# Performance work log

Measured on AMD Instinct MI355X. Metric: run time of the kernel, lower is better.

Reference implementation:

```python
import jax, jax.numpy as jnp
import numpy as np
import math

NUM_CLASSES = 15
IN_CH = 256
FEAT_CH = 256
STRIDES = (8, 16, 32, 64, 128)
SCALES = (4.0,)
RATIOS = (6.0,)
ANGLES = (-0.125 * math.pi, 0.125 * math.pi, 0.375 * math.pi, 0.625 * math.pi)
NUM_ANCHORS = len(SCALES) * len(RATIOS) * len(ANGLES)  # 4
WH_RATIO_CLIP = 1e-6


def conv2d(x, w, b, pad):
    y = jax.lax.conv_general_dilated(
        x, w, window_strides=(1, 1), padding=[(pad, pad), (pad, pad)],
        dimension_numbers=("NCHW", "OIHW", "NCHW"))
    return y + b[None, :, None, None]


def gen_grid_anchors(base_size, feat_h, feat_w, stride):
    # AnchorGeneratorRotated (S2ANet style): base anchors [A,5] = (xc,yc,w,h,angle)
    scales = jnp.asarray(SCALES, jnp.float32)
    ratios = jnp.asarray(RATIOS, jnp.float32)
    angles = jnp.asarray(ANGLES, jnp.float32)
    h_ratios = jnp.sqrt(ratios)
    w_ratios = 1.0 / h_ratios
    ones = jnp.ones_like(angles)
    ws = (base_size * w_ratios[:, None, None] * scales[None, :, None] * ones[None, None, :]).reshape(-1)
    hs = (base_size * h_ratios[:, None, None] * scales[None, :, None] * ones[None, None, :]).reshape(-1)
    ang = jnp.tile(angles, ratios.size * scales.size)
    ctr = 0.5 * (base_size - 1.0)
    base = jnp.stack([jnp.full_like(ws, ctr), jnp.full_like(ws, ctr), ws, hs, ang], axis=-1)  # [A,5]
    xx = jnp.arange(feat_w, dtype=jnp.float32) * stride
    yy = jnp.arange(feat_h, dtype=jnp.float32) * stride
    gx, gy = jnp.meshgrid(xx, yy)  # [H,W]
    zeros = jnp.zeros_like(gx)
    shift = jnp.stack([gx, gy, zeros, zeros, zeros], axis=-1)  # [H,W,5]
    return base[None, None] + shift[:, :, None, :]  # [H,W,A,5]


def norm_angle(a):
    # normalize to [-pi/4, 3pi/4)
    return (a + 0.25 * jnp.pi) % jnp.pi - 0.25 * jnp.pi


def rboxes_decode(anchors, deltas):
    # is_encode_relative=False branch of delta2rbox
    max_ratio = abs(math.log(WH_RATIO_CLIP))
    dx, dy, dw, dh, da = jnp.split(deltas, 5, axis=-1)
    rx, ry, rw, rh, ra = jnp.split(anchors, 5, axis=-1)
    dw = jnp.clip(dw, -max_ratio, max_ratio)
    dh = jnp.clip(dh, -max_ratio, max_ratio)
    gx = dx * rw + rx
    gy = dy * rh + ry
    gw = rw * jnp.exp(dw)
    gh = rh * jnp.exp(dh)
    ga = norm_angle(da + ra)
    return jnp.concatenate([gx, gy, gw, gh, ga], axis=-1)


def _head_level(x, stride, p):
    B, _, H, W = x.shape
    # reg tower (2 stacked 3x3 conv + relu)
    r = jax.nn.relu(conv2d(x, p["reg_w0"], p["reg_b0"], 1))
    r = jax.nn.relu(conv2d(r, p["reg_w1"], p["reg_b1"], 1))
    bbox = conv2d(r, p["reg_head_w"], p["reg_head_b"], 0)
    bbox = bbox.transpose(0, 2, 3, 1).reshape(B, H, W, NUM_ANCHORS, 5)
    conf = conv2d(r, p["conf_w"], p["conf_b"], 0)
    conf = conf.transpose(0, 2, 3, 1).reshape(B, H, W, NUM_ANCHORS, 1)
    anchors = gen_grid_anchors(float(stride), H, W, float(stride))  # [H,W,A,5]
    dec = rboxes_decode(anchors[None], jax.lax.stop_gradient(bbox))  # [B,H,W,A,5]
    # refine-anchor selection: pick decoded box of max-confidence anchor per location
    conf_sig = jax.nn.sigmoid(jax.lax.stop_gradient(conf))[..., 0]  # [B,H,W,A]
    idx = jnp.argmax(conf_sig, axis=3)  # [B,H,W]
    refine = jnp.take_along_axis(dec, idx[..., None, None], axis=3)[:, :, :, 0, :]  # [B,H,W,5]
    # cls tower
    c = jax.nn.relu(conv2d(x, p["cls_w0"], p["cls_b0"], 1))
    c = jax.nn.relu(conv2d(c, p["cls_w1"], p["cls_b1"], 1))
    cls = conv2d(c, p["cls_head_w"], p["cls_head_b"], 0)
    cls = cls.transpose(0, 2, 3, 1).reshape(B, H, W, NUM_ANCHORS, NUM_CLASSES)
    # per-image scores as in get_bboxes: sigmoid(cls) * sigmoid(conf)
    scores = jax.nn.sigmoid(cls.reshape(B, -1, NUM_CLASSES)) * jax.nn.sigmoid(conf.reshape(B, -1, 1))
    return scores, dec.reshape(B, -1, 5), refine


def setup_inputs() -> dict:
    key = jax.random.key(0)
    ks = jax.random.split(key, 24)
    B = 8
    sizes = [(128, 128), (64, 64), (32, 32), (16, 16), (8, 8)]
    inp = {}
    for i, (h, w) in enumerate(sizes):
        inp[f"feat{i}"] = jax.random.normal(ks[i], (B, IN_CH, h, w), jnp.float32)
    std = 0.01
    bias_cls = float(-np.log((1 - 0.01) / 0.01))
    inp["reg_w0"] = jax.random.normal(ks[5], (FEAT_CH, IN_CH, 3, 3), jnp.float32) * std
    inp["reg_b0"] = jnp.zeros((FEAT_CH,), jnp.float32)
    inp["reg_w1"] = jax.random.normal(ks[6], (FEAT_CH, FEAT_CH, 3, 3), jnp.float32) * std
    inp["reg_b1"] = jnp.zeros((FEAT_CH,), jnp.float32)
    inp["cls_w0"] = jax.random.normal(ks[7], (FEAT_CH, IN_CH, 3, 3), jnp.float32) * std
    inp["cls_b0"] = jnp.zeros((FEAT_CH,), jnp.float32)
    inp["cls_w1"] = jax.random.normal(ks[8], (FEAT_CH, FEAT_CH, 3, 3), jnp.float32) * std
    inp["cls_b1"] = jnp.zeros((FEAT_CH,), jnp.float32)
    inp["reg_head_w"] = jax.random.normal(ks[9], (5 * NUM_ANCHORS, FEAT_CH, 1, 1), jnp.float32) * std
    inp["reg_head_b"] = jnp.zeros((5 * NUM_ANCHORS,), jnp.float32)
    inp["cls_head_w"] = jax.random.normal(ks[10], (NUM_CLASSES * NUM_ANCHORS, FEAT_CH, 1, 1), jnp.float32) * std
    inp["cls_head_b"] = jnp.full((NUM_CLASSES * NUM_ANCHORS,), bias_cls, jnp.float32)
    inp["conf_w"] = jax.random.normal(ks[11], (NUM_ANCHORS, FEAT_CH, 1, 1), jnp.float32) * std
    inp["conf_b"] = jnp.full((NUM_ANCHORS,), bias_cls, jnp.float32)
    return inp


def reference(feat0, feat1, feat2, feat3, feat4,
              reg_w0, reg_b0, reg_w1, reg_b1,
              cls_w0, cls_b0, cls_w1, cls_b1,
              reg_head_w, reg_head_b, cls_head_w, cls_head_b,
              conf_w, conf_b):
    p = dict(reg_w0=reg_w0, reg_b0=reg_b0, reg_w1=reg_w1, reg_b1=reg_b1,
             cls_w0=cls_w0, cls_b0=cls_b0, cls_w1=cls_w1, cls_b1=cls_b1,
             reg_head_w=reg_head_w, reg_head_b=reg_head_b,
             cls_head_w=cls_head_w, cls_head_b=cls_head_b,
             conf_w=conf_w, conf_b=conf_b)
    feats = [feat0, feat1, feat2, feat3, feat4]
    scores_ls, boxes_ls = [], []
    for x, s in zip(feats, STRIDES):
        sc, bx, _ = _head_level(x, s, p)
        scores_ls.append(sc)
        boxes_ls.append(bx)
    scores = jnp.concatenate(scores_ls, axis=1)  # [B, N_total, num_classes]
    boxes = jnp.concatenate(boxes_ls, axis=1)    # [B, N_total, 5]
    return scores, boxes
```

## Files before the change

kernel.cpp:

```cpp
#include <hip/hip_runtime.h>


typedef __attribute__((ext_vector_type(8))) _Float16 f16x8;
typedef __attribute__((ext_vector_type(4))) float f32x4;

#define SCORES_TOTAL 10475520ull

__device__ __forceinline__ unsigned short f2h(float f) {
  union { _Float16 h; unsigned short u; } x;
  x.h = (_Float16)f;
  return x.u;
}

__device__ __forceinline__ float sigmf(float x) {
  return 1.0f / (1.0f + expf(-x));
}

__device__ __forceinline__ void gload_lds16(const unsigned short* g,
                                            unsigned short* l) {
  __builtin_amdgcn_global_load_lds(
      (const __attribute__((address_space(1))) unsigned int*)g,
      (__attribute__((address_space(3))) unsigned int*)l, 16, 0, 0);
}

__device__ __forceinline__ void lvl_lookup(int gm, int& logW, int& mbase) {
  if (gm < 131072) { logW = 7; mbase = 0; }
  else if (gm < 163840) { logW = 6; mbase = 131072; }
  else if (gm < 172032) { logW = 5; mbase = 163840; }
  else if (gm < 174080) { logW = 4; mbase = 172032; }
  else { logW = 3; mbase = 174080; }
}

__global__ __launch_bounds__(256) void prep_convw(
    const float* __restrict__ w0, const float* __restrict__ w1,
    const float* __restrict__ w2, const float* __restrict__ w3,
    unsigned short* __restrict__ wtout) {
  int g = blockIdx.x * 256 + threadIdx.x;
  int q = g >> 16;
  int wsel = q / 9;
  int kk = q - wsel * 9;
  int r = g & 65535;
  int oc = r >> 8, ic = r & 255;
  const float* src = (wsel == 0) ? w0 : (wsel == 1) ? w1 : (wsel == 2) ? w2 : w3;
  float v = src[(size_t)(oc * 256 + ic) * 9 + kk];
  wtout[(size_t)wsel * 589824 + (size_t)((kk << 8) + oc) * 256 + ic] = f2h(v);
}

__global__ __launch_bounds__(256) void prep_small(
    const float* __restrict__ clsh, const float* __restrict__ regh,
    const float* __restrict__ confw,
    unsigned short* __restrict__ wc, unsigned short* __restrict__ wh,
    unsigned short* __restrict__ zp) {
  int g = blockIdx.x * 256 + threadIdx.x;
  if (g < 16384) {
    int row = g >> 8, ic = g & 255;
    float v = (row < 60) ? clsh[row * 256 + ic] : 0.0f;
    wc[g] = f2h(v);
  } else if (g < 24576) {
    int gg = g - 16384;
    int row = gg >> 8, ic = gg & 255;
    float v = 0.0f;
    if (row < 20) v = regh[row * 256 + ic];
    else if (row < 24) v = confw[(row - 20) * 256 + ic];
    wh[gg] = f2h(v);
  } else if (g < 24640) {
    zp[g - 24576] = 0;
  }
}

__global__ __launch_bounds__(256) void to_nhwc_all(
    const float* __restrict__ f0, const float* __restrict__ f1,
    const float* __restrict__ f2, const float* __restrict__ f3,
    const float* __restrict__ f4, unsigned short* __restrict__ out) {
  __shared__ unsigned short L[64][258];
  const int t = threadIdx.x;
  const int gm0 = blockIdx.x * 64;
  int logW, mbase;
  const float* in;
  if (gm0 < 131072) { logW = 7; mbase = 0; in = f0; }
  else if (gm0 < 163840) { logW = 6; mbase = 131072; in = f1; }
  else if (gm0 < 172032) { logW = 5; mbase = 163840; in = f2; }
  else if (gm0 < 174080) { logW = 4; mbase = 172032; in = f3; }
  else { logW = 3; mbase = 174080; in = f4; }
  const int logHW = 2 * logW;
  const int HW = 1 << logHW;
  const int lm0 = gm0 - mbase;
  const int b = lm0 >> logHW;
  const int hw0 = lm0 & (HW - 1);
#pragma unroll
  for (int it = 0; it < 16; ++it) {
    int c = it * 16 + (t >> 4);
    int j4 = (t & 15) * 4;
    float4 v = *reinterpret_cast<const float4*>(
        in + (size_t)(b * 256 + c) * HW + hw0 + j4);
    L[j4 + 0][c] = f2h(v.x);
    L[j4 + 1][c] = f2h(v.y);
    L[j4 + 2][c] = f2h(v.z);
    L[j4 + 3][c] = f2h(v.w);
  }
  __syncthreads();
#pragma unroll
  for (int it = 0; it < 16; ++it) {
    int j = it * 4 + (t >> 6);
    int c4 = (t & 63) * 4;
    unsigned v0 = (unsigned)L[j][c4 + 0] | ((unsigned)L[j][c4 + 1] << 16);
    unsigned v1 = (unsigned)L[j][c4 + 2] | ((unsigned)L[j][c4 + 3] << 16);
    uint2 v = make_uint2(v0, v1);
    *reinterpret_cast<uint2*>(out + ((size_t)(gm0 + j) << 8) + c4) = v;
  }
}

__global__ __launch_bounds__(256, 2) void conv1f(
    const unsigned short* __restrict__ xin,
    const unsigned short* __restrict__ wtR,
    const unsigned short* __restrict__ wtC,
    const float* __restrict__ biasR, const float* __restrict__ biasC,
    const unsigned short* __restrict__ zp,
    unsigned short* __restrict__ outR,
    unsigned short* __restrict__ outC, int gm_base) {
  __shared__ unsigned short pool[24576];
  const int t = threadIdx.x;
  const int lane = t & 63;
  const int wv = t >> 6;
  const int wm = wv >> 1, wn = wv & 1;
  const int gm0 = gm_base + blockIdx.x * 128;
  const int n0 = blockIdx.y << 7;
  int logW, mbase;
  lvl_lookup(gm0, logW, mbase);
  const int logHW = 2 * logW;
  const int H = 1 << logW, W = H;
  const int HWm1 = (1 << logHW) - 1, Wm1 = W - 1;

  const int srow = lane >> 2;
  const int schk = (((lane & 3) ^ ((lane >> 3) & 3)) << 3);
  int hjj[2], wjj[2];
  const unsigned short* aptrj[2];
  const unsigned short* bRj[2];
  const unsigned short* bCj[2];
  const int sldrow = (wv << 5);
#pragma unroll
  for (int j = 0; j < 2; ++j) {
    int gm = gm0 + sldrow + (j << 4) + srow;
    int lm = gm - mbase;
    int hw = lm & HWm1;
    hjj[j] = hw >> logW;
    wjj[j] = hw & Wm1;
    aptrj[j] = xin + ((size_t)gm << 8) + schk;
    int br = n0 + sldrow + (j << 4) + srow;
    bRj[j] = wtR + ((size_t)br << 8) + schk;
    bCj[j] = wtC + ((size_t)br << 8) + schk;
  }

  f32x4 accR[4][4], accC[4][4];
#pragma unroll
  for (int i = 0; i < 4; ++i)
#pragma unroll
    for (int j = 0; j < 4; ++j) {
      accR[i][j] = (f32x4){0.f, 0.f, 0.f, 0.f};
      accC[i][j] = (f32x4){0.f, 0.f, 0.f, 0.f};
    }

  const int arow = (wm << 6) + (lane & 15);
  const int brow = (wn << 6) + (lane & 15);
  const int sxor = ((lane & 15) >> 1) & 3;
  const int achk = (((lane >> 4) ^ sxor) << 3);

  {
    const int moff = (-W - 1) << 8;
#pragma unroll
    for (int j = 0; j < 2; ++j) {
      bool valid = (hjj[j] > 0) & (wjj[j] > 0);
      const unsigned short* g = valid ? (aptrj[j] + moff) : zp;
      gload_lds16(g, pool + ((sldrow + (j << 4)) << 5));
    }
#pragma unroll
    for (int j = 0; j < 2; ++j) {
      gload_lds16(bRj[j], pool + 8192 + ((sldrow + (j << 4)) << 5));
      gload_lds16(bCj[j], pool + 16384 + ((sldrow + (j << 4)) << 5));
    }
  }

  int cur = 0;
#pragma unroll 1
  for (int ph = 0; ph < 72; ++ph) {
    asm volatile("s_waitcnt vmcnt(0)" ::: "memory");
    __builtin_amdgcn_s_barrier();
    __builtin_amdgcn_sched_barrier(0);
    if (ph < 71) {
      const int p = ph + 1;
      const int kk = p >> 3;
      const int k3 = kk / 3;
      const int dy = k3 - 1, dxv = kk - k3 * 3 - 1;
      const int moff = ((dy << logW) + dxv) << 8;
      const int ic0 = (p & 7) << 5;
      const int nb = (cur ^ 1) << 12;
      const int bko = (kk << 16) + ic0;
#pragma unroll
      for (int j = 0; j < 2; ++j) {
        bool valid = ((unsigned)(hjj[j] + dy) < (unsigned)H) &
                     ((unsigned)(wjj[j] + dxv) < (unsigned)W);
        const unsigned short* g = valid ? (aptrj[j] + moff + ic0) : zp;
        gload_lds16(g, pool + nb + ((sldrow + (j << 4)) << 5));
      }
#pragma unroll
      for (int j = 0; j < 2; ++j) {
        gload_lds16(bRj[j] + bko, pool + 8192 + nb + ((sldrow + (j << 4)) << 5));
        gload_lds16(bCj[j] + bko, pool + 16384 + nb + ((sldrow + (j << 4)) << 5));
      }
    }
    const int cb = cur << 12;
    f16x8 a[4], bR[4], bC[4];
#pragma unroll
    for (int mf = 0; mf < 4; ++mf)
      a[mf] = *reinterpret_cast<const f16x8*>(
          pool + cb + ((arow + (mf << 4)) << 5) + achk);
#pragma unroll
    for (int nf = 0; nf < 4; ++nf) {
      bR[nf] = *reinterpret_cast<const f16x8*>(
          pool + 8192 + cb + ((brow + (nf << 4)) << 5) + achk);
      bC[nf] = *reinterpret_cast<const f16x8*>(
          pool + 16384 + cb + ((brow + (nf << 4)) << 5) + achk);
    }
#pragma unroll
    for (int mf = 0; mf < 4; ++mf)
#pragma unroll
      for (int nf = 0; nf < 4; ++nf) {
        accR[mf][nf] = __builtin_amdgcn_mfma_f32_16x16x32_f16(
            a[mf], bR[nf], accR[mf][nf], 0, 0, 0);
        accC[mf][nf] = __builtin_amdgcn_mfma_f32_16x16x32_f16(
            a[mf], bC[nf], accC[mf][nf], 0, 0, 0);
      }
    cur ^= 1;
  }
  __syncthreads();

  const int erow = t >> 1;
  const int ech = t & 1;
  const unsigned short* esrc =
      pool + ((((erow >> 6) << 1) + ech) << 12) + ((erow & 63) << 6);
  unsigned short* ep = pool + (wv << 12);
  const int eg = (lane >> 4) << 2;
  const int el = lane & 15;
  const int lrow0 = gm0 - gm_base;

#pragma unroll
  for (int nf = 0; nf < 4; ++nf) {
    float bi = biasR[n0 + (wn << 6) + (nf << 4) + el];
#pragma unroll
    for (int mf = 0; mf < 4; ++mf)
#pragma unroll
      for (int r = 0; r < 4; ++r)
        ep[((mf << 4) + eg + r) * 64 + (nf << 4) + el] =
            f2h(fmaxf(accR[mf][nf][r] + bi, 0.0f));
  }
  __syncthreads();
  {
    unsigned short* edst =
        outR + ((size_t)(lrow0 + erow) << 8) + n0 + (ech << 6);
#pragma unroll
    for (int q = 0; q < 8; ++q)
      reinterpret_cast<uint4*>(edst)[q] =
          reinterpret_cast<const uint4*>(esrc)[q];
  }
  __syncthreads();
#pragma unroll
  for (int nf = 0; nf < 4; ++nf) {
    float bi = biasC[n0 + (wn << 6) + (nf << 4) + el];
#pragma unroll
    for (int mf = 0; mf < 4; ++mf)
#pragma unroll
      for (int r = 0; r < 4; ++r)
        ep[((mf << 4) + eg + r) * 64 + (nf << 4) + el] =
            f2h(fmaxf(accC[mf][nf][r] + bi, 0.0f));
  }
  __syncthreads();
  {
    unsigned short* edst =
        outC + ((size_t)(lrow0 + erow) << 8) + n0 + (ech << 6);
#pragma unroll
    for (int q = 0; q < 8; ++q)
      reinterpret_cast<uint4*>(edst)[q] =
          reinterpret_cast<const uint4*>(esrc)[q];
  }
}

__global__ __launch_bounds__(256, 2) void conv2w(
    const unsigned short* __restrict__ xin,
    const unsigned short* __restrict__ wt,
    const float* __restrict__ bias,
    const unsigned short* __restrict__ zp,
    unsigned short* __restrict__ yout,
    int gm_base) {
  __shared__ unsigned short pool[24576];
  const int t = threadIdx.x;
  const int lane = t & 63;
  const int wv = t >> 6;
  const int wm = wv >> 1, wn = wv & 1;
  const int gm0 = gm_base + blockIdx.x * 128;
  int logW, mbase;
  lvl_lookup(gm0, logW, mbase);
  const int logHW = 2 * logW;
  const int H = 1 << logW, W = H;
  const int HWm1 = (1 << logHW) - 1, Wm1 = W - 1;

  const int srow = lane >> 2;
  const int schk = (((lane & 3) ^ ((lane >> 3) & 3)) << 3);
  int hjj[2], wjj[2];
  const unsigned short* aptrj[2];
  const int sldrow = (wv << 5);
#pragma unroll
  for (int j = 0; j < 2; ++j) {
    int gm = gm0 + sldrow + (j << 4) + srow;
    int lm = gm - mbase;
    int hw = lm & HWm1;
    hjj[j] = hw >> logW;
    wjj[j] = hw & Wm1;
    aptrj[j] = xin + ((size_t)(gm - gm_base) << 8) + schk;
  }
  const unsigned short* bpj[4];
#pragma unroll
  for (int j = 0; j < 4; ++j) {
    int row = (wv << 6) + (j << 4) + srow;
    bpj[j] = wt + ((size_t)row << 8) + schk;
  }

  f32x4 acc[4][8];
#pragma unroll
  for (int i = 0; i < 4; ++i)
#pragma unroll
    for (int j = 0; j < 8; ++j) acc[i][j] = (f32x4){0.f, 0.f, 0.f, 0.f};

  const int arow = (wm << 6) + (lane & 15);
  const int brow = (wn << 7) + (lane & 15);
  const int sxor = ((lane & 15) >> 1) & 3;
  const int achk = (((lane >> 4) ^ sxor) << 3);

  {
    const int moff = (-W - 1) << 8;
#pragma unroll
    for (int j = 0; j < 2; ++j) {
      bool valid = (hjj[j] > 0) & (wjj[j] > 0);
      const unsigned short* g = valid ? (aptrj[j] + moff) : zp;
      gload_lds16(g, pool + ((sldrow + (j << 4)) << 5));
    }
#pragma unroll
    for (int j = 0; j < 4; ++j)
      gload_lds16(bpj[j], pool + 8192 + (((wv << 6) + (j << 4)) << 5));
  }

  int cur = 0;
#pragma unroll 1
  for (int ph = 0; ph < 72; ++ph) {
    asm volatile("s_waitcnt vmcnt(0)" ::: "memory");
    __builtin_amdgcn_s_barrier();
    __builtin_amdgcn_sched_barrier(0);
    if (ph < 71) {
      const int p = ph + 1;
      const int kk = p >> 3;
      const int k3 = kk / 3;
      const int dy = k3 - 1, dxv = kk - k3 * 3 - 1;
      const int moff = ((dy << logW) + dxv) << 8;
      const int ic0 = (p & 7) << 5;
      const int bko = (kk << 16) + ic0;
#pragma unroll
      for (int j = 0; j < 2; ++j) {
        bool valid = ((unsigned)(hjj[j] + dy) < (unsigned)H) &
                     ((unsigned)(wjj[j] + dxv) < (unsigned)W);
        const unsigned short* g = valid ? (aptrj[j] + moff + ic0) : zp;
        gload_lds16(g, pool + ((cur ^ 1) << 12) + ((sldrow + (j << 4)) << 5));
      }
#pragma unroll
      for (int j = 0; j < 4; ++j)
        gload_lds16(bpj[j] + bko, pool + 8192 + ((cur ^ 1) << 13) +
                                      (((wv << 6) + (j << 4)) << 5));
    }
    const int cbA = cur << 12;
    const int cbB = cur << 13;
    f16x8 a[4], b[8];
#pragma unroll
    for (int mf = 0; mf < 4; ++mf)
      a[mf] = *reinterpret_cast<const f16x8*>(
          pool + cbA + ((arow + (mf << 4)) << 5) + achk);
#pragma unroll
    for (int nf = 0; nf < 8; ++nf)
      b[nf] = *reinterpret_cast<const f16x8*>(
          pool + 8192 + cbB + ((brow + (nf << 4)) << 5) + achk);
#pragma unroll
    for (int mf = 0; mf < 4; ++mf)
#pragma unroll
      for (int nf = 0; nf < 8; ++nf)
        acc[mf][nf] = __builtin_amdgcn_mfma_f32_16x16x32_f16(
            a[mf], b[nf], acc[mf][nf], 0, 0, 0);
    cur ^= 1;
  }
  __syncthreads();

  const int erow = t >> 1;
  const int ech = t & 1;
  const unsigned short* esrc =
      pool + ((((erow >> 6) << 1) + ech) << 12) + ((erow & 63) << 6);
  unsigned short* ep = pool + (wv << 12);
  const int eg = (lane >> 4) << 2;
  const int el = lane & 15;

#pragma unroll
  for (int h = 0; h < 2; ++h) {
    if (h) __syncthreads();
#pragma unroll
    for (int q4 = 0; q4 < 4; ++q4) {
      int nf = (h << 2) + q4;
      float bi = bias[(wn << 7) + (nf << 4) + el];
#pragma unroll
      for (int mf = 0; mf < 4; ++mf)
#pragma unroll
        for (int r = 0; r < 4; ++r)
          ep[((mf << 4) + eg + r) * 64 + (q4 << 4) + el] =
              f2h(fmaxf(acc[mf][nf][r] + bi, 0.0f));
    }
    __syncthreads();
    unsigned short* edst =
        yout + ((size_t)(gm0 + erow) << 8) + (ech << 7) + (h << 6);
#pragma unroll
    for (int q = 0; q < 8; ++q)
      reinterpret_cast<uint4*>(edst)[q] =
          reinterpret_cast<const uint4*>(esrc)[q];
  }
}

__global__ __launch_bounds__(256) void head24_mfma(
    const unsigned short* __restrict__ t2,
    const unsigned short* __restrict__ wh,
    const float* __restrict__ regb, const float* __restrict__ confb,
    float* __restrict__ hbuf) {
  const int t = threadIdx.x, lane = t & 63, wv = t >> 6;
  const int rowb = blockIdx.x * 256 + wv * 64;
  const int kgrp = (lane >> 4) << 3;
  const int l15 = lane & 15;
  f32x4 acc[4][2];
#pragma unroll
  for (int i = 0; i < 4; ++i)
#pragma unroll
    for (int j = 0; j < 2; ++j) acc[i][j] = (f32x4){0.f, 0.f, 0.f, 0.f};
#pragma unroll
  for (int k0 = 0; k0 < 256; k0 += 32) {
    f16x8 a[4], b[2];
#pragma unroll
    for (int mf = 0; mf < 4; ++mf)
      a[mf] = *reinterpret_cast<const f16x8*>(
          t2 + (((size_t)(rowb + (mf << 4) + l15)) << 8) + k0 + kgrp);
#pragma unroll
    for (int nf = 0; nf < 2; ++nf)
      b[nf] = *reinterpret_cast<const f16x8*>(
          wh + (size_t)(((nf << 4) + l15) << 8) + k0 + kgrp);
#pragma unroll
    for (int mf = 0; mf < 4; ++mf)
#pragma unroll
      for (int nf = 0; nf < 2; ++nf)
        acc[mf][nf] = __builtin_amdgcn_mfma_f32_16x16x32_f16(
            a[mf], b[nf], acc[mf][nf], 0, 0, 0);
  }
#pragma unroll
  for (int nf = 0; nf < 2; ++nf) {
    int c = (nf << 4) + l15;
    if (c < 24) {
      float bi = (c < 20) ? regb[c] : confb[c - 20];
#pragma unroll
      for (int mf = 0; mf < 4; ++mf)
#pragma unroll
        for (int r = 0; r < 4; ++r) {
          int m = rowb + (mf << 4) + ((lane >> 4) << 2) + r;
          hbuf[(size_t)m * 24 + c] = acc[mf][nf][r] + bi;
        }
    }
  }
}

__global__ __launch_bounds__(256) void cls_scores(
    const unsigned short* __restrict__ t2,
    const unsigned short* __restrict__ wcw,
    const float* __restrict__ clsb,
    const float* __restrict__ hbuf,
    float* __restrict__ outs, int gm_base) {
  const int t = threadIdx.x, lane = t & 63, wv = t >> 6;
  const int gm0 = gm_base + blockIdx.x * 256;
  int logW, mbase, lvl_off;
  if (gm0 < 131072) { logW = 7; mbase = 0; lvl_off = 0; }
  else if (gm0 < 163840) { logW = 6; mbase = 131072; lvl_off = 65536; }
  else if (gm0 < 172032) { logW = 5; mbase = 163840; lvl_off = 81920; }
  else if (gm0 < 174080) { logW = 4; mbase = 172032; lvl_off = 86016; }
  else { logW = 3; mbase = 174080; lvl_off = 87040; }
  const int logHW = 2 * logW, HWm1 = (1 << logHW) - 1;
  const int rowb = gm0 + wv * 64;
  const int kgrp = (lane >> 4) << 3;
  const int l15 = lane & 15;
  f32x4 acc[4][4];
#pragma unroll
  for (int i = 0; i < 4; ++i)
#pragma unroll
    for (int j = 0; j < 4; ++j) acc[i][j] = (f32x4){0.f, 0.f, 0.f, 0.f};
#pragma unroll
  for (int k0 = 0; k0 < 256; k0 += 32) {
    f16x8 a[4], b[4];
#pragma unroll
    for (int mf = 0; mf < 4; ++mf)
      a[mf] = *reinterpret_cast<const f16x8*>(
          t2 + (((size_t)(rowb + (mf << 4) + l15)) << 8) + k0 + kgrp);
#pragma unroll
    for (int nf = 0; nf < 4; ++nf)
      b[nf] = *reinterpret_cast<const f16x8*>(
          wcw + (size_t)(((nf << 4) + l15) << 8) + k0 + kgrp);
#pragma unroll
    for (int mf = 0; mf < 4; ++mf)
#pragma unroll
      for (int nf = 0; nf < 4; ++nf)
        acc[mf][nf] = __builtin_amdgcn_mfma_f32_16x16x32_f16(
            a[mf], b[nf], acc[mf][nf], 0, 0, 0);
  }
#pragma unroll
  for (int nf = 0; nf < 4; ++nf) {
    int c = (nf << 4) + l15;
    if (c < 60) {
      int ai = c / 15, ci = c - ai * 15;
      float bi = clsb[c];
#pragma unroll
      for (int mf = 0; mf < 4; ++mf)
#pragma unroll
        for (int r = 0; r < 4; ++r) {
          int m = rowb + (mf << 4) + ((lane >> 4) << 2) + r;
          float logit = acc[mf][nf][r] + bi;
          float conf = hbuf[(size_t)m * 24 + 20 + ai];
          float sc = sigmf(logit) * sigmf(conf);
          int lm = m - mbase;
          int b = lm >> logHW;
          int hw = lm & HWm1;
          int loc = lvl_off + (hw << 2) + ai;
          outs[(size_t)b * 1309440 + (size_t)loc * 15 + ci] = sc;
        }
    }
  }
}

__global__ __launch_bounds__(256) void decode_all(
    const float* __restrict__ hbuf, float* __restrict__ outb) {
  int tid = blockIdx.x * 256 + threadIdx.x;
  if (tid >= 174592 * 4) return;
  int m = tid >> 2, a = tid & 3;
  int logW, mbase, lvl_off;
  float stride;
  if (m < 131072) { logW = 7; mbase = 0; lvl_off = 0; stride = 8.f; }
  else if (m < 163840) { logW = 6; mbase = 131072; lvl_off = 65536; stride = 16.f; }
  else if (m < 172032) { logW = 5; mbase = 163840; lvl_off = 81920; stride = 32.f; }
  else if (m < 174080) { logW = 4; mbase = 172032; lvl_off = 86016; stride = 64.f; }
  else { logW = 3; mbase = 174080; lvl_off = 87040; stride = 128.f; }
  const int logHW = 2 * logW;
  const float ANG[4] = {-0.39269908169872414f, 0.39269908169872414f,
                        1.1780972450961724f, 1.9634954084936207f};
  const float* d = hbuf + (size_t)m * 24 + a * 5;
  float dx = d[0], dy = d[1], dw = d[2], dh = d[3], da = d[4];
  int lm = m - mbase;
  int b = lm >> logHW, hw = lm & ((1 << logHW) - 1);
  int h = hw >> logW, w = hw & ((1 << logW) - 1);
  float ctr = 0.5f * (stride - 1.0f);
  float rx = w * stride + ctr, ry = h * stride + ctr;
  float rw = stride * 1.6329931618554521f;
  float rh = stride * 9.7979589711327124f;
  const float MR = 13.815510557964274f;
  dw = fminf(fmaxf(dw, -MR), MR);
  dh = fminf(fmaxf(dh, -MR), MR);
  float gx = dx * rw + rx;
  float gy = dy * rh + ry;
  float gw = rw * expf(dw);
  float gh = rh * expf(dh);
  float v = da + ANG[a] + 0.7853981633974483f;
  float r = fmodf(v, 3.14159265358979323846f);
  if (r < 0.0f) r += 3.14159265358979323846f;
  float ga = r - 0.7853981633974483f;
  int loc = lvl_off + (hw << 2) + a;
  size_t base = (size_t)b * 436480 + (size_t)loc * 5;
  outb[base + 0] = gx;
  outb[base + 1] = gy;
  outb[base + 2] = gw;
  outb[base + 3] = gh;
  outb[base + 4] = ga;
}

extern "C" void kernel_launch(void* const* d_in, const int* in_sizes, int n_in,
                              void* d_out, int out_size, void* d_ws,
                              size_t ws_size, hipStream_t stream) {
  const float* feats[5];
  for (int i = 0; i < 5; ++i) feats[i] = (const float*)d_in[i];
  const float* reg_w0 = (const float*)d_in[5];
  const float* reg_b0 = (const float*)d_in[6];
  const float* reg_w1 = (const float*)d_in[7];
  const float* reg_b1 = (const float*)d_in[8];
  const float* cls_w0 = (const float*)d_in[9];
  const float* cls_b0 = (const float*)d_in[10];
  const float* cls_w1 = (const float*)d_in[11];
  const float* cls_b1 = (const float*)d_in[12];
  const float* reg_head_w = (const float*)d_in[13];
  const float* reg_head_b = (const float*)d_in[14];
  const float* cls_head_w = (const float*)d_in[15];
  const float* cls_head_b = (const float*)d_in[16];
  const float* conf_w = (const float*)d_in[17];
  const float* conf_b = (const float*)d_in[18];

  unsigned short* ws = (unsigned short*)d_ws;
  unsigned short* t1r = ws + 44695552ull;
  unsigned short* t1c = ws + 78249984ull;
  unsigned short* wt4 = ws + 111804416ull;
  unsigned short* wh = ws + 114163712ull;
  unsigned short* wc = ws + 114171904ull;
  unsigned short* zp = ws + 114188288ull;
  float* hbuf_all = (float*)((char*)d_ws + 228376704ull);

  prep_convw<<<9216, 256, 0, stream>>>(reg_w0, reg_w1, cls_w0, cls_w1, wt4);
  prep_small<<<97, 256, 0, stream>>>(cls_head_w, reg_head_w, conf_w, wc, wh,
                                     zp);
  to_nhwc_all<<<2728, 256, 0, stream>>>(feats[0], feats[1], feats[2], feats[3],
                                        feats[4], ws);

  float* scores = (float*)d_out;
  float* boxes = (float*)d_out + SCORES_TOTAL;

  static const int gbase[2] = {0, 131072};
  static const int gM[2] = {131072, 43520};
  for (int g = 0; g < 2; ++g) {
    const int base = gbase[g];
    const int M = gM[g];
    conv1f<<<dim3(M / 128, 2), 256, 0, stream>>>(
        ws, wt4 + 0ull * 589824, wt4 + 2ull * 589824, reg_b0, cls_b0, zp, t1r,
        t1c, base);
    conv2w<<<M / 128, 256, 0, stream>>>(t1r, wt4 + 1ull * 589824, reg_b1, zp,
                                        ws, base);
    head24_mfma<<<M / 256, 256, 0, stream>>>(
        ws + ((size_t)base << 8), wh, reg_head_b, conf_b,
        hbuf_all + (size_t)base * 24);
    conv2w<<<M / 128, 256, 0, stream>>>(t1c, wt4 + 3ull * 589824, cls_b1, zp,
                                        ws, base);
    cls_scores<<<M / 256, 256, 0, stream>>>(ws, wc, cls_head_b, hbuf_all,
                                            scores, base);
  }
  decode_all<<<(174592 * 4 + 255) / 256, 256, 0, stream>>>(hbuf_all, boxes);
}
```

Baseline: 1.182 ms.

## Triple-buffer LDS staging with prefetch distance two in conv kernels

```diff
diff --git a/kernel.cpp b/kernel.cpp
--- a/kernel.cpp
+++ b/kernel.cpp
@@ -118,7 +118,7 @@
     const unsigned short* __restrict__ zp,
     unsigned short* __restrict__ outR,
     unsigned short* __restrict__ outC, int gm_base) {
-  __shared__ unsigned short pool[24576];
+  __shared__ unsigned short pool[36864];
   const int t = threadIdx.x;
   const int lane = t & 63;
   const int wv = t >> 6;
@@ -163,52 +163,47 @@
   const int arow = (wm << 6) + (lane & 15);
   const int brow = (wn << 6) + (lane & 15);
   const int sxor = ((lane & 15) >> 1) & 3;
-  const int achk = (((lane >> 4) ^ sxor) << 3);
-
-  {
-    const int moff = (-W - 1) << 8;
+  const int achk = (((lane >> 4) << 3)) ^ (sxor << 3);
+
+  auto STAGE = [&](int p, int buf) {
+    int icp = p / 9;
+    int kk = p - icp * 9;
+    int k3 = kk / 3;
+    int dy = k3 - 1, dxv = kk - k3 * 3 - 1;
+    int moff = ((dy << logW) + dxv) << 8;
+    int ic0 = icp << 5;
+    int bko = (kk << 16) + ic0;
+    const int ab = buf << 12;
 #pragma unroll
     for (int j = 0; j < 2; ++j) {
-      bool valid = (hjj[j] > 0) & (wjj[j] > 0);
-      const unsigned short* g = valid ? (aptrj[j] + moff) : zp;
-      gload_lds16(g, pool + ((sldrow + (j << 4)) << 5));
+      bool valid = ((unsigned)(hjj[j] + dy) < (unsigned)H) &
+                   ((unsigned)(wjj[j] + dxv) < (unsigned)W);
+      const unsigned short* g = valid ? (aptrj[j] + moff + ic0) : zp;
+      gload_lds16(g, pool + ab + ((sldrow + (j << 4)) << 5));
     }
 #pragma unroll
     for (int j = 0; j < 2; ++j) {
-      gload_lds16(bRj[j], pool + 8192 + ((sldrow + (j << 4)) << 5));
-      gload_lds16(bCj[j], pool + 16384 + ((sldrow + (j << 4)) << 5));
-    }
-  }
-
-  int cur = 0;
+      gload_lds16(bRj[j] + bko, pool + 12288 + ab + ((sldrow + (j << 4)) << 5));
+      gload_lds16(bCj[j] + bko, pool + 24576 + ab + ((sldrow + (j << 4)) << 5));
+    }
+  };
+
+  STAGE(0, 0);
+  STAGE(1, 1);
+
+  int cbuf = 0;
 #pragma unroll 1
   for (int ph = 0; ph < 72; ++ph) {
-    asm volatile("s_waitcnt vmcnt(0)" ::: "memory");
+    if (ph < 71) asm volatile("s_waitcnt vmcnt(6)" ::: "memory");
+    else         asm volatile("s_waitcnt vmcnt(0)" ::: "memory");
     __builtin_amdgcn_s_barrier();
     __builtin_amdgcn_sched_barrier(0);
-    if (ph < 71) {
-      const int p = ph + 1;
-      const int kk = p >> 3;
-      const int k3 = kk / 3;
-      const int dy = k3 - 1, dxv = kk - k3 * 3 - 1;
-      const int moff = ((dy << logW) + dxv) << 8;
-      const int ic0 = (p & 7) << 5;
-      const int nb = (cur ^ 1) << 12;
-      const int bko = (kk << 16) + ic0;
-#pragma unroll
-      for (int j = 0; j < 2; ++j) {
-        bool valid = ((unsigned)(hjj[j] + dy) < (unsigned)H) &
-                     ((unsigned)(wjj[j] + dxv) < (unsigned)W);
-        const unsigned short* g = valid ? (aptrj[j] + moff + ic0) : zp;
-        gload_lds16(g, pool + nb + ((sldrow + (j << 4)) << 5));
-      }
-#pragma unroll
-      for (int j = 0; j < 2; ++j) {
-        gload_lds16(bRj[j] + bko, pool + 8192 + nb + ((sldrow + (j << 4)) << 5));
-        gload_lds16(bCj[j] + bko, pool + 16384 + nb + ((sldrow + (j << 4)) << 5));
-      }
-    }
-    const int cb = cur << 12;
+    if (ph < 70) {
+      int sb = cbuf + 2; if (sb >= 3) sb -= 3;
+      STAGE(ph + 2, sb);
+    }
+    __builtin_amdgcn_sched_barrier(0);
+    const int cb = cbuf << 12;
     f16x8 a[4], bR[4], bC[4];
 #pragma unroll
     for (int mf = 0; mf < 4; ++mf)
@@ -217,9 +212,9 @@
 #pragma unroll
     for (int nf = 0; nf < 4; ++nf) {
       bR[nf] = *reinterpret_cast<const f16x8*>(
-          pool + 8192 + cb + ((brow + (nf << 4)) << 5) + achk);
+          pool + 12288 + cb + ((brow + (nf << 4)) << 5) + achk);
       bC[nf] = *reinterpret_cast<const f16x8*>(
-          pool + 16384 + cb + ((brow + (nf << 4)) << 5) + achk);
+          pool + 24576 + cb + ((brow + (nf << 4)) << 5) + achk);
     }
 #pragma unroll
     for (int mf = 0; mf < 4; ++mf)
@@ -230,7 +225,7 @@
         accC[mf][nf] = __builtin_amdgcn_mfma_f32_16x16x32_f16(
             a[mf], bC[nf], accC[mf][nf], 0, 0, 0);
       }
-    cur ^= 1;
+    cbuf = (cbuf == 2) ? 0 : cbuf + 1;
   }
   __syncthreads();
 
@@ -291,7 +286,7 @@
     const unsigned short* __restrict__ zp,
     unsigned short* __restrict__ yout,
     int gm_base) {
-  __shared__ unsigned short pool[24576];
+  __shared__ unsigned short pool[36864];
   const int t = threadIdx.x;
   const int lane = t & 63;
   const int wv = t >> 6;
@@ -333,49 +328,46 @@
   const int arow = (wm << 6) + (lane & 15);
   const int brow = (wn << 7) + (lane & 15);
   const int sxor = ((lane & 15) >> 1) & 3;
-  const int achk = (((lane >> 4) ^ sxor) << 3);
-
-  {
-    const int moff = (-W - 1) << 8;
+  const int achk = (((lane >> 4) << 3)) ^ (sxor << 3);
+
+  auto STAGE = [&](int p, int buf) {
+    int icp = p / 9;
+    int kk = p - icp * 9;
+    int k3 = kk / 3;
+    int dy = k3 - 1, dxv = kk - k3 * 3 - 1;
+    int moff = ((dy << logW) + dxv) << 8;
+    int ic0 = icp << 5;
+    int bko = (kk << 16) + ic0;
 #pragma unroll
     for (int j = 0; j < 2; ++j) {
-      bool valid = (hjj[j] > 0) & (wjj[j] > 0);
-      const unsigned short* g = valid ? (aptrj[j] + moff) : zp;
-      gload_lds16(g, pool + ((sldrow + (j << 4)) << 5));
+      bool valid = ((unsigned)(hjj[j] + dy) < (unsigned)H) &
+                   ((unsigned)(wjj[j] + dxv) < (unsigned)W);
+      const unsigned short* g = valid ? (aptrj[j] + moff + ic0) : zp;
+      gload_lds16(g, pool + (buf << 12) + ((sldrow + (j << 4)) << 5));
     }
 #pragma unroll
     for (int j = 0; j < 4; ++j)
-      gload_lds16(bpj[j], pool + 8192 + (((wv << 6) + (j << 4)) << 5));
-  }
-
-  int cur = 0;
+      gload_lds16(bpj[j] + bko, pool + 12288 + (buf << 13) +
+                                    (((wv << 6) + (j << 4)) << 5));
+  };
+
+  STAGE(0, 0);
+  STAGE(1, 1);
+
+  int cbuf = 0;
 #pragma unroll 1
   for (int ph = 0; ph < 72; ++ph) {
-    asm volatile("s_waitcnt vmcnt(0)" ::: "memory");
+    if (ph < 71) asm volatile("s_waitcnt vmcnt(6)" ::: "memory");
+    else         asm volatile("s_waitcnt vmcnt(0)" ::: "memory");
     __builtin_amdgcn_s_barrier();
     __builtin_amdgcn_sched_barrier(0);
-    if (ph < 71) {
-      const int p = ph + 1;
-      const int kk = p >> 3;
-      const int k3 = kk / 3;
-      const int dy = k3 - 1, dxv = kk - k3 * 3 - 1;
-      const int moff = ((dy << logW) + dxv) << 8;
-      const int ic0 = (p & 7) << 5;
-      const int bko = (kk << 16) + ic0;
-#pragma unroll
-      for (int j = 0; j < 2; ++j) {
-        bool valid = ((unsigned)(hjj[j] + dy) < (unsigned)H) &
-                     ((unsigned)(wjj[j] + dxv) < (unsigned)W);
-        const unsigned short* g = valid ? (aptrj[j] + moff + ic0) : zp;
-        gload_lds16(g, pool + ((cur ^ 1) << 12) + ((sldrow + (j << 4)) << 5));
-      }
-#pragma unroll
-      for (int j = 0; j < 4; ++j)
-        gload_lds16(bpj[j] + bko, pool + 8192 + ((cur ^ 1) << 13) +
-                                      (((wv << 6) + (j << 4)) << 5));
-    }
-    const int cbA = cur << 12;
-    const int cbB = cur << 13;
+    if (ph < 70) {
+      int sb = cbuf + 2; if (sb >= 3) sb -= 3;
+      STAGE(ph + 2, sb);
+    }
+    __builtin_amdgcn_sched_barrier(0);
+    const int cbA = cbuf << 12;
+    const int cbB = cbuf << 13;
     f16x8 a[4], b[8];
 #pragma unroll
     for (int mf = 0; mf < 4; ++mf)
@@ -384,14 +376,14 @@
 #pragma unroll
     for (int nf = 0; nf < 8; ++nf)
       b[nf] = *reinterpret_cast<const f16x8*>(
-          pool + 8192 + cbB + ((brow + (nf << 4)) << 5) + achk);
+          pool + 12288 + cbB + ((brow + (nf << 4)) << 5) + achk);
 #pragma unroll
     for (int mf = 0; mf < 4; ++mf)
 #pragma unroll
       for (int nf = 0; nf < 8; ++nf)
         acc[mf][nf] = __builtin_amdgcn_mfma_f32_16x16x32_f16(
             a[mf], b[nf], acc[mf][nf], 0, 0, 0);
-    cur ^= 1;
+    cbuf = (cbuf == 2) ? 0 : cbuf + 1;
   }
   __syncthreads();
 
```

Result: faster. 1.115 ms (-5.7%).
